# Optimization experiments

Hardware: AMD Instinct MI355X
Metric: run time of the kernel (lower is better)

The kernel has to match this reference:

```python
import jax, jax.numpy as jnp
import numpy as np

DIM = 1024
HEADS = 16
RADIUS = 4


def setup_inputs() -> dict:
    key = jax.random.key(0)
    ks = jax.random.split(key, 5)
    B, T, D = 4, 2048, DIM
    s = 1.0 / np.sqrt(D)
    x = jax.random.normal(ks[0], (B, T, D), dtype=jnp.float32)
    w_qkv = jax.random.uniform(ks[1], (3 * D, D), minval=-s, maxval=s, dtype=jnp.float32)
    b_qkv = jax.random.uniform(ks[2], (3 * D,), minval=-s, maxval=s, dtype=jnp.float32)
    w_proj = jax.random.uniform(ks[3], (D, D), minval=-s, maxval=s, dtype=jnp.float32)
    b_proj = jax.random.uniform(ks[4], (D,), minval=-s, maxval=s, dtype=jnp.float32)
    return {"x": x, "w_qkv": w_qkv, "b_qkv": b_qkv, "w_proj": w_proj, "b_proj": b_proj}


def reference(x, w_qkv, b_qkv, w_proj, b_proj):
    B, T, D = x.shape
    H = HEADS
    hd = D // H
    scale = hd ** -0.5
    qkv = x @ w_qkv.T + b_qkv                       # [B,T,3D]
    qkv = qkv.reshape(B, T, 3, H, hd).transpose(2, 0, 3, 1, 4)  # [3,B,H,T,hd]
    q, k, v = qkv[0], qkv[1], qkv[2]
    attn = jnp.einsum('bhqd,bhkd->bhqk', q, k) * scale  # [B,H,T,T]
    idx = jnp.arange(T)
    mask = jnp.abs(idx[None, :] - idx[:, None]) > RADIUS  # [T,T]
    attn = jnp.where(mask[None, None], -jnp.inf, attn)
    attn = jax.nn.softmax(attn, axis=-1)
    out = jnp.einsum('bhqk,bhkd->bhqd', attn, v)    # [B,H,T,hd]
    out = out.transpose(0, 2, 1, 3).reshape(B, T, D)
    return out @ w_proj.T + b_proj
```

## Files before the change

### kernel.cpp

```cpp
#include <hip/hip_runtime.h>
#include <hip/hip_bf16.h>
#include <cstdint>
#include <cstddef>
#include <type_traits>


typedef __hip_bfloat16 bf16;
typedef __attribute__((ext_vector_type(8))) short bf16x8;
typedef __attribute__((ext_vector_type(4))) float f32x4;
typedef __attribute__((ext_vector_type(8))) unsigned short u16x8;

#define BATCH  4
#define SEQ    2048
#define DIM    1024
#define NHEAD  16
#define HDIM   64
#define RADIUS 4
#define ROWS   (BATCH * SEQ)
#define KDIM   1024
#define HSLICE (SEQ * HDIM)

__device__ __forceinline__ void async_copy16(const void* gptr, void* lptr) {
    __builtin_amdgcn_global_load_lds(
        (const __attribute__((address_space(1))) unsigned int*)(uintptr_t)gptr,
        (__attribute__((address_space(3))) unsigned int*)(uint32_t)(uintptr_t)lptr,
        16, 0, 0);
}

__global__ __launch_bounds__(256)
void cvt_all(const float* __restrict__ s1, bf16* __restrict__ d1, int n1,
             const float* __restrict__ s2, bf16* __restrict__ d2, int n2,
             const float* __restrict__ s3, bf16* __restrict__ d3, int n3) {
    int i = blockIdx.x * blockDim.x + threadIdx.x;
    const float* src; bf16* dst;
    if (i < n1)              { src = s1; dst = d1; }
    else if (i < n1 + n2)    { i -= n1; src = s2; dst = d2; }
    else if (i < n1+n2+n3)   { i -= n1 + n2; src = s3; dst = d3; }
    else return;
    const float4 a = ((const float4*)src)[2 * i];
    const float4 b = ((const float4*)src)[2 * i + 1];
    union { u16x8 v; __hip_bfloat16 h[8]; } o;
    o.h[0] = __float2bfloat16(a.x); o.h[1] = __float2bfloat16(a.y);
    o.h[2] = __float2bfloat16(a.z); o.h[3] = __float2bfloat16(a.w);
    o.h[4] = __float2bfloat16(b.x); o.h[5] = __float2bfloat16(b.y);
    o.h[6] = __float2bfloat16(b.z); o.h[7] = __float2bfloat16(b.w);
    ((u16x8*)dst)[i] = o.v;
}

template <int NMAT, typename OutT, bool QKV_LAYOUT>
__device__ __forceinline__
void gemm_body(const bf16* __restrict__ A, const bf16* __restrict__ B,
               const float* __restrict__ bias, OutT* __restrict__ C) {
    __shared__ bf16 As[128 * 64];
    __shared__ bf16 Bs[128 * 64];

    const int tid  = threadIdx.x;
    const int lane = tid & 63;
    const int wave = tid >> 6;
    const int quad = lane >> 4;
    const int l16  = lane & 15;

    const int tileM = blockIdx.y * 128;
    const int tileN = blockIdx.x * 128;
    const int wm = (wave >> 1) * 64;
    const int wn = (wave & 1) * 64;

    f32x4 acc[4][4] = {};

    for (int kt = 0; kt < KDIM; kt += 64) {
        #pragma unroll
        for (int i = 0; i < 4; ++i) {
            const int c   = i * 256 + tid;
            const int row = c >> 3;
            const int kg  = (c & 7) ^ (row & 7);
            async_copy16(A + (size_t)(tileM + row) * KDIM + kt + kg * 8,
                         (char*)As + c * 16);
            async_copy16(B + (size_t)(tileN + row) * KDIM + kt + kg * 8,
                         (char*)Bs + c * 16);
        }
        __syncthreads();

        #pragma unroll
        for (int ks = 0; ks < 2; ++ks) {
            const int kq = ks * 4 + quad;
            const int so = (kq ^ (l16 & 7)) * 8;
            bf16x8 aF[4], bF[4];
            #pragma unroll
            for (int mt = 0; mt < 4; ++mt)
                aF[mt] = *(const bf16x8*)(As + (wm + mt * 16 + l16) * 64 + so);
            #pragma unroll
            for (int nt = 0; nt < 4; ++nt)
                bF[nt] = *(const bf16x8*)(Bs + (wn + nt * 16 + l16) * 64 + so);

            #pragma unroll
            for (int mt = 0; mt < 4; ++mt)
                #pragma unroll
                for (int nt = 0; nt < 4; ++nt)
                    acc[mt][nt] = __builtin_amdgcn_mfma_f32_16x16x32_bf16(
                        aF[mt], bF[nt], acc[mt][nt], 0, 0, 0);
        }
        __syncthreads();
    }

    #pragma unroll
    for (int nt = 0; nt < 4; ++nt) {
        const int scol = tileN + wn + nt * 16;
        const float bv = bias[scol + l16];
        #pragma unroll
        for (int mt = 0; mt < 4; ++mt) {
            #pragma unroll
            for (int r = 0; r < 4; ++r) {
                const int rowg = tileM + wm + mt * 16 + quad * 4 + r;
                const float v = acc[mt][nt][r] + bv;
                if constexpr (QKV_LAYOUT) {
                    const int s = scol >> 10;
                    const int h = (scol >> 6) & (NHEAD - 1);
                    const int d = (scol & 63) + l16;
                    const int b = rowg >> 11;
                    const int t = rowg & (SEQ - 1);
                    ((bf16*)C)[(size_t)((b * NHEAD + h) * 3 + s) * HSLICE
                               + (size_t)t * HDIM + d] = __float2bfloat16(v);
                } else if constexpr (std::is_same<OutT, float>::value) {
                    C[(size_t)rowg * NMAT + scol + l16] = v;
                } else {
                    C[(size_t)rowg * NMAT + scol + l16] = __float2bfloat16(v);
                }
            }
        }
    }
}

__global__ __launch_bounds__(256)
void gemm_qkv(const bf16* __restrict__ A, const bf16* __restrict__ B,
              const float* __restrict__ bias, bf16* __restrict__ C) {
    gemm_body<3072, bf16, true>(A, B, bias, C);
}

__global__ __launch_bounds__(256)
void gemm_proj(const bf16* __restrict__ A, const bf16* __restrict__ B,
               const float* __restrict__ bias, float* __restrict__ C) {
    gemm_body<1024, float, false>(A, B, bias, C);
}

__device__ __forceinline__ void bf8_to_f32(const uint4 u, float* f) {
    union { uint32_t u; float f; } c;
    c.u = u.x << 16;         f[0] = c.f;
    c.u = u.x & 0xffff0000u; f[1] = c.f;
    c.u = u.y << 16;         f[2] = c.f;
    c.u = u.y & 0xffff0000u; f[3] = c.f;
    c.u = u.z << 16;         f[4] = c.f;
    c.u = u.z & 0xffff0000u; f[5] = c.f;
    c.u = u.w << 16;         f[6] = c.f;
    c.u = u.w & 0xffff0000u; f[7] = c.f;
}

__global__ __launch_bounds__(256)
void attn_banded4(const bf16* __restrict__ qkv, bf16* __restrict__ aout) {
    const int tid = threadIdx.x;
    const int qi  = tid >> 2;
    const int ch  = tid & 3;
    const int t   = blockIdx.x * 64 + qi;
    const int h   = blockIdx.y;
    const int b   = blockIdx.z;

    const size_t bh3 = (size_t)(b * NHEAD + h) * 3;
    const bf16* qb = qkv + (bh3 + 0) * HSLICE + (size_t)t * HDIM + ch * 16;
    const bf16* kb = qkv + (bh3 + 1) * HSLICE + ch * 16;
    const bf16* vb = qkv + (bh3 + 2) * HSLICE + ch * 16;
    const float scale = 0.125f;

    float q16[16];
    {
        const uint4* qp = (const uint4*)qb;
        uint4 u0 = qp[0], u1 = qp[1];
        bf8_to_f32(u0, q16); bf8_to_f32(u1, q16 + 8);
    }

    float sc[2 * RADIUS + 1];
    #pragma unroll
    for (int j = 0; j < 2 * RADIUS + 1; ++j) {
        const int k = t - RADIUS + j;
        const bool valid = (k >= 0) && (k < SEQ);
        const int kc = valid ? k : t;
        const uint4* kp = (const uint4*)(kb + (size_t)kc * HDIM);
        float kf[16];
        uint4 u0 = kp[0], u1 = kp[1];
        bf8_to_f32(u0, kf); bf8_to_f32(u1, kf + 8);
        float p = 0.f;
        #pragma unroll
        for (int e = 0; e < 16; ++e) p = fmaf(q16[e], kf[e], p);
        p += __shfl_xor(p, 1, 64);
        p += __shfl_xor(p, 2, 64);
        sc[j] = valid ? p * scale : -1e30f;
    }

    float mx = sc[0];
    #pragma unroll
    for (int j = 1; j < 2 * RADIUS + 1; ++j) mx = fmaxf(mx, sc[j]);
    float sum = 0.f;
    #pragma unroll
    for (int j = 0; j < 2 * RADIUS + 1; ++j) { sc[j] = __expf(sc[j] - mx); sum += sc[j]; }
    const float inv = 1.0f / sum;

    float o16[16];
    #pragma unroll
    for (int e = 0; e < 16; ++e) o16[e] = 0.f;
    #pragma unroll
    for (int j = 0; j < 2 * RADIUS + 1; ++j) {
        const int k = t - RADIUS + j;
        const int kc = (k >= 0 && k < SEQ) ? k : t;
        const uint4* vp = (const uint4*)(vb + (size_t)kc * HDIM);
        float vf[16];
        uint4 u0 = vp[0], u1 = vp[1];
        bf8_to_f32(u0, vf); bf8_to_f32(u1, vf + 8);
        const float w = sc[j];
        #pragma unroll
        for (int e = 0; e < 16; ++e) o16[e] = fmaf(w, vf[e], o16[e]);
    }

    bf16* op = aout + ((size_t)b * SEQ + t) * DIM + h * HDIM + ch * 16;
    #pragma unroll
    for (int c2 = 0; c2 < 2; ++c2) {
        union { u16x8 v; __hip_bfloat16 hh[8]; } o;
        #pragma unroll
        for (int e = 0; e < 8; ++e) o.hh[e] = __float2bfloat16(o16[c2 * 8 + e] * inv);
        ((u16x8*)op)[c2] = o.v;
    }
}

extern "C" void kernel_launch(void* const* d_in, const int* in_sizes, int n_in,
                              void* d_out, int out_size, void* d_ws, size_t ws_size,
                              hipStream_t stream) {
    const float* x      = (const float*)d_in[0];
    const float* w_qkv  = (const float*)d_in[1];
    const float* b_qkv  = (const float*)d_in[2];
    const float* w_proj = (const float*)d_in[3];
    const float* b_proj = (const float*)d_in[4];
    float* out = (float*)d_out;

    bf16* xb     = (bf16*)d_ws;
    bf16* wqkvb  = xb + (size_t)ROWS * DIM;
    bf16* wprojb = wqkvb + (size_t)3072 * 1024;
    bf16* qkvb   = wprojb + (size_t)1024 * 1024;
    bf16* attnb  = qkvb + (size_t)ROWS * 3072;

    const int n1 = ROWS * DIM / 8, n2 = 3072 * 1024 / 8, n3 = 1024 * 1024 / 8;
    cvt_all<<<(n1 + n2 + n3 + 255) / 256, 256, 0, stream>>>(x, xb, n1, w_qkv, wqkvb, n2,
                                                            w_proj, wprojb, n3);

    gemm_qkv<<<dim3(3072 / 128, ROWS / 128), 256, 0, stream>>>(xb, wqkvb, b_qkv, qkvb);

    attn_banded4<<<dim3(SEQ / 64, NHEAD, BATCH), 256, 0, stream>>>(qkvb, attnb);

    gemm_proj<<<dim3(1024 / 128, ROWS / 128), 256, 0, stream>>>(attnb, wprojb, b_proj, out);
}
```

Measured before the change: 201.0 us.

## Replace QKV GEMM with 256x256-tile, 8-wave, double-buffered pipelined kernel

```diff
diff --git a/kernel.cpp b/kernel.cpp
--- a/kernel.cpp
+++ b/kernel.cpp
@@ -18,6 +18,7 @@
 #define RADIUS 4
 #define ROWS   (BATCH * SEQ)
 #define KDIM   1024
+#define NT     (KDIM / 64)
 #define HSLICE (SEQ * HDIM)
 
 __device__ __forceinline__ void async_copy16(const void* gptr, void* lptr) {
@@ -47,7 +48,160 @@
     ((u16x8*)dst)[i] = o.v;
 }
 
-template <int NMAT, typename OutT, bool QKV_LAYOUT>
+
+#define PHB() do {                                  \
+    asm volatile("" ::: "memory");                  \
+    __builtin_amdgcn_sched_barrier(0);              \
+    __builtin_amdgcn_s_barrier();                   \
+    __builtin_amdgcn_sched_barrier(0);              \
+    asm volatile("" ::: "memory");                  \
+} while (0)
+
+#define STAGE_A(buf_, half_, kt_) do {                                          \
+    _Pragma("unroll")                                                           \
+    for (int i_ = 0; i_ < 2; ++i_) {                                            \
+        const int c_   = i_ * 512 + tid;                                        \
+        const int row_ = (half_) * 128 + (c_ >> 3);                             \
+        const int kg_  = (c_ & 7) ^ (row_ & 7);                                 \
+        async_copy16(A + (size_t)(tileM + row_) * KDIM + (kt_) + kg_ * 8,       \
+                     (char*)As[buf_] + ((half_) * 1024 + c_) * 16);             \
+    } } while (0)
+
+#define STAGE_B(buf_, half_, kt_) do {                                          \
+    _Pragma("unroll")                                                           \
+    for (int i_ = 0; i_ < 2; ++i_) {                                            \
+        const int c_   = i_ * 512 + tid;                                        \
+        const int row_ = (half_) * 128 + (c_ >> 3);                             \
+        const int kg_  = (c_ & 7) ^ (row_ & 7);                                 \
+        async_copy16(B + (size_t)(tileN + row_) * KDIM + (kt_) + kg_ * 8,       \
+                     (char*)Bs[buf_] + ((half_) * 1024 + c_) * 16);             \
+    } } while (0)
+
+#define LDA_Q(mh_) do {                                                         \
+    _Pragma("unroll")                                                           \
+    for (int ks_ = 0; ks_ < 2; ++ks_)                                           \
+    _Pragma("unroll")                                                           \
+    for (int mt_ = 0; mt_ < 4; ++mt_)                                           \
+        aF[ks_][mt_] = *(const bf16x8*)(as_ +                                   \
+            (size_t)(wm * 128 + (mh_) * 64 + mt_ * 16 + l16) * 64 +             \
+            ((((ks_ << 2) | quad) ^ hh) << 3));                                 \
+} while (0)
+
+#define LDB_Q(BF_, nh_) do {                                                    \
+    _Pragma("unroll")                                                           \
+    for (int ks_ = 0; ks_ < 2; ++ks_)                                           \
+    _Pragma("unroll")                                                           \
+    for (int nt_ = 0; nt_ < 2; ++nt_)                                           \
+        BF_[ks_][nt_] = *(const bf16x8*)(bs_ +                                  \
+            (size_t)(wn * 64 + (nh_) * 32 + nt_ * 16 + l16) * 64 +              \
+            ((((ks_ << 2) | quad) ^ hh) << 3));                                 \
+} while (0)
+
+#define MFMA_Q(mh_, nh_, BF_) do {                                              \
+    _Pragma("unroll")                                                           \
+    for (int ks_ = 0; ks_ < 2; ++ks_)                                           \
+    _Pragma("unroll")                                                           \
+    for (int mt_ = 0; mt_ < 4; ++mt_)                                           \
+    _Pragma("unroll")                                                           \
+    for (int nt_ = 0; nt_ < 2; ++nt_)                                           \
+        acc[(mh_) * 4 + mt_][(nh_) * 2 + nt_] =                                 \
+            __builtin_amdgcn_mfma_f32_16x16x32_bf16(                            \
+                aF[ks_][mt_], BF_[ks_][nt_],                                    \
+                acc[(mh_) * 4 + mt_][(nh_) * 2 + nt_], 0, 0, 0);                \
+} while (0)
+
+__global__ __launch_bounds__(512, 1)
+void gemm_qkv_8p(const bf16* __restrict__ A, const bf16* __restrict__ B,
+                 const float* __restrict__ bias, bf16* __restrict__ C) {
+    __shared__ bf16 As[2][256 * 64];
+    __shared__ bf16 Bs[2][256 * 64];
+
+    const int tid  = threadIdx.x;
+    const int l16  = tid & 15;
+    const int quad = (tid >> 4) & 3;
+    const int wave = tid >> 6;
+    const int wm   = wave >> 2;
+    const int wn   = wave & 3;
+    const int hh   = l16 & 7;
+
+    int bid = (int)blockIdx.x;
+    bid = (bid & 7) * 48 + (bid >> 3);
+    const int tileM = (bid / 12) * 256;
+    const int tileN = (bid % 12) * 256;
+
+    f32x4  acc[8][4] = {};
+    bf16x8 aF[2][4], bF0[2][2], bF1[2][2];
+
+    STAGE_A(0, 0, 0);  STAGE_B(0, 0, 0);  STAGE_A(0, 1, 0);  STAGE_B(0, 1, 0);
+    STAGE_A(1, 0, 64); STAGE_B(1, 0, 64); STAGE_A(1, 1, 64); STAGE_B(1, 1, 64);
+    asm volatile("s_waitcnt vmcnt(8)" ::: "memory");
+    PHB();
+
+    #pragma unroll 1
+    for (int t = 0; t < NT; ++t) {
+        const int buf = t & 1;
+        const bf16* __restrict__ as_ = &As[buf][0];
+        const bf16* __restrict__ bs_ = &Bs[buf][0];
+        const int  kt2 = (t + 2) * 64;
+        const bool pf  = (t + 2 < NT);
+
+        LDA_Q(0);
+        LDB_Q(bF0, 0);
+        PHB();
+        __builtin_amdgcn_s_setprio(1);
+        MFMA_Q(0, 0, bF0);
+        __builtin_amdgcn_s_setprio(0);
+        PHB();
+
+        LDB_Q(bF1, 1);
+        PHB();
+        __builtin_amdgcn_s_setprio(1);
+        MFMA_Q(0, 1, bF1);
+        __builtin_amdgcn_s_setprio(0);
+        PHB();
+
+        LDA_Q(1);
+        if (pf) { STAGE_B(buf, 0, kt2); STAGE_B(buf, 1, kt2); }
+        PHB();
+        __builtin_amdgcn_s_setprio(1);
+        MFMA_Q(1, 1, bF1);
+        __builtin_amdgcn_s_setprio(0);
+        PHB();
+
+        if (pf) { STAGE_A(buf, 0, kt2); STAGE_A(buf, 1, kt2); }
+        PHB();
+        __builtin_amdgcn_s_setprio(1);
+        MFMA_Q(1, 0, bF0);
+        __builtin_amdgcn_s_setprio(0);
+        if (pf)                 asm volatile("s_waitcnt vmcnt(8)" ::: "memory");
+        else if (t + 1 < NT)    asm volatile("s_waitcnt vmcnt(0)" ::: "memory");
+        PHB();
+    }
+
+    #pragma unroll
+    for (int an = 0; an < 4; ++an) {
+        const int scol = tileN + wn * 64 + an * 16;
+        const int cl   = scol + l16;
+        const float bv = bias[cl];
+        const int s = cl >> 10;
+        const int h = (cl >> 6) & (NHEAD - 1);
+        const int d = cl & 63;
+        #pragma unroll
+        for (int am = 0; am < 8; ++am) {
+            #pragma unroll
+            for (int r = 0; r < 4; ++r) {
+                const int rowg = tileM + wm * 128 + am * 16 + quad * 4 + r;
+                const int b  = rowg >> 11;
+                const int tt = rowg & (SEQ - 1);
+                C[(size_t)((b * NHEAD + h) * 3 + s) * HSLICE
+                  + (size_t)tt * HDIM + d] =
+                    __float2bfloat16(acc[am][an][r] + bv);
+            }
+        }
+    }
+}
+
+template <int NMAT, typename OutT>
 __device__ __forceinline__
 void gemm_body(const bf16* __restrict__ A, const bf16* __restrict__ B,
                const float* __restrict__ bias, OutT* __restrict__ C) {
@@ -112,34 +266,16 @@
             for (int r = 0; r < 4; ++r) {
                 const int rowg = tileM + wm + mt * 16 + quad * 4 + r;
                 const float v = acc[mt][nt][r] + bv;
-                if constexpr (QKV_LAYOUT) {
-                    const int s = scol >> 10;
-                    const int h = (scol >> 6) & (NHEAD - 1);
-                    const int d = (scol & 63) + l16;
-                    const int b = rowg >> 11;
-                    const int t = rowg & (SEQ - 1);
-                    ((bf16*)C)[(size_t)((b * NHEAD + h) * 3 + s) * HSLICE
-                               + (size_t)t * HDIM + d] = __float2bfloat16(v);
-                } else if constexpr (std::is_same<OutT, float>::value) {
-                    C[(size_t)rowg * NMAT + scol + l16] = v;
-                } else {
-                    C[(size_t)rowg * NMAT + scol + l16] = __float2bfloat16(v);
-                }
+                C[(size_t)rowg * NMAT + scol + l16] = v;
             }
         }
     }
-}
-
-__global__ __launch_bounds__(256)
-void gemm_qkv(const bf16* __restrict__ A, const bf16* __restrict__ B,
-              const float* __restrict__ bias, bf16* __restrict__ C) {
-    gemm_body<3072, bf16, true>(A, B, bias, C);
 }
 
 __global__ __launch_bounds__(256)
 void gemm_proj(const bf16* __restrict__ A, const bf16* __restrict__ B,
                const float* __restrict__ bias, float* __restrict__ C) {
-    gemm_body<1024, float, false>(A, B, bias, C);
+    gemm_body<1024, float>(A, B, bias, C);
 }
 
 __device__ __forceinline__ void bf8_to_f32(const uint4 u, float* f) {
@@ -248,7 +384,7 @@
     cvt_all<<<(n1 + n2 + n3 + 255) / 256, 256, 0, stream>>>(x, xb, n1, w_qkv, wqkvb, n2,
                                                             w_proj, wprojb, n3);
 
-    gemm_qkv<<<dim3(3072 / 128, ROWS / 128), 256, 0, stream>>>(xb, wqkvb, b_qkv, qkvb);
+    gemm_qkv_8p<<<dim3(384), 512, 0, stream>>>(xb, wqkvb, b_qkv, qkvb);
 
     attn_banded4<<<dim3(SEQ / 64, NHEAD, BATCH), 256, 0, stream>>>(qkvb, attnb);
 
```

Result: slower. 210.8 us (+4.9%).
